# Performance work log

Hardware: AMD Instinct MI355X
Metric: run time of the kernel (lower is better)

Reference implementation:

```python
import jax, jax.numpy as jnp
import numpy as np

D = 256  # feature_dim
NQ = 512
NK = 512


def setup_inputs() -> dict:
    key = jax.random.key(0)
    ks = jax.random.split(key, 12)
    s = 0.05
    return {
        "x": jax.random.normal(ks[0], (1, D, NQ), dtype=jnp.float32),
        "source": jax.random.normal(ks[1], (1, D, NK), dtype=jnp.float32),
        "dist": jax.random.normal(ks[2], (1, D, NQ * NK), dtype=jnp.float32),
        "mask": jax.random.randint(ks[3], (NQ, NK), 0, 2).astype(jnp.bool_),
        # MLPAttention mlp: channels [3D, D, 1] (1x1 convs == per-position matmuls)
        "aW1": jax.random.normal(ks[4], (D, 3 * D), dtype=jnp.float32) * s,
        "ab1": jax.random.normal(ks[5], (D,), dtype=jnp.float32) * s,
        "aW2": jax.random.normal(ks[6], (1, D), dtype=jnp.float32) * s,
        "ab2": jax.random.normal(ks[7], (1,), dtype=jnp.float32) * s,
        # merge mlp: channels [2D, 2D, D], last bias initialized to 0
        "mW1": jax.random.normal(ks[8], (2 * D, 2 * D), dtype=jnp.float32) * s,
        "mb1": jax.random.normal(ks[9], (2 * D,), dtype=jnp.float32) * s,
        "mW2": jax.random.normal(ks[10], (D, 2 * D), dtype=jnp.float32) * s,
        "mb2": jnp.zeros((D,), dtype=jnp.float32),
    }


def _conv1x1(W, b, x):
    # Conv1d(kernel_size=1): (out,in) @ (b,in,n) -> (b,out,n)
    return jnp.einsum('oc,bcn->bon', W, x) + b[None, :, None]


def reference(x, source, dist, mask, aW1, ab1, aW2, ab2, mW1, mb1, mW2, mb2):
    nq, nk = x.shape[-1], source.shape[-1]
    d = x.shape[1]
    # broadcast query over keys and key over queries, flatten to (1, d, nq*nk)
    qb = jnp.broadcast_to(x[:, :, :, None], (1, d, nq, nk)).reshape(1, d, nq * nk)
    kb = jnp.broadcast_to(source[:, :, None, :], (1, d, nq, nk)).reshape(1, d, nq * nk)
    feat = jnp.concatenate([qb, kb, dist], axis=1)  # (1, 3d, nq*nk)
    h = jax.nn.relu(_conv1x1(aW1, ab1, feat))       # (1, d, nq*nk)
    scores = _conv1x1(aW2, ab2, h).reshape(1, nq, nk)
    # boolean-mask branch: push masked-out entries far below the min
    neg = jax.lax.stop_gradient(scores.min()) - 20.0
    scores = scores + neg * (~mask).astype(scores.dtype)[None]
    prob = jax.nn.softmax(scores, axis=-1)
    message = jnp.einsum('bnm,bdm->bdn', prob, source)  # value == source
    # merge MLP on concat([x, message])
    cat = jnp.concatenate([x, message], axis=1)  # (1, 2d, nq)
    h2 = jax.nn.relu(_conv1x1(mW1, mb1, cat))
    out = _conv1x1(mW2, mb2, h2)  # (1, d, nq)
    return (out, scores)
```

## Files before the change

kernel.cpp:

```cpp
#include <hip/hip_runtime.h>
#include <stdint.h>

#define D_ 256
#define NQ_ 512
#define NK_ 512
#define NP_ (NQ_*NK_)

typedef __attribute__((ext_vector_type(8))) __bf16 bf16x8;
typedef __attribute__((ext_vector_type(4))) float f32x4;

__device__ __forceinline__ unsigned short f2bf(float f) {
  unsigned u = __builtin_bit_cast(unsigned, f);
  u += 0x7FFFu + ((u >> 16) & 1u);
  return (unsigned short)(u >> 16);
}
__device__ __forceinline__ unsigned encf(float f) {
  unsigned u = __builtin_bit_cast(unsigned, f);
  return (u & 0x80000000u) ? ~u : (u | 0x80000000u);
}
__device__ __forceinline__ float decf(unsigned e) {
  unsigned u = (e & 0x80000000u) ? (e ^ 0x80000000u) : ~e;
  return __builtin_bit_cast(float, u);
}

template<int EPI, int KTILES>
__device__ __forceinline__ void gemm_body(
    const unsigned short* __restrict__ A, int lda,
    const unsigned short* __restrict__ B, int ldb,
    const float* __restrict__ bias,
    void* __restrict__ Dst, int ldd, int nTilesN, int bid) {
  const int t = threadIdx.x, w = t >> 6, l = t & 63, l15 = l & 15, g = l >> 4;
  const int bm = bid / nTilesN, bn = bid % nTilesN;
  const int m0 = bm*64 + w*16, n0 = bn*64;
  const unsigned short* Ap = A + (size_t)(m0 + l15)*lda + g*8;
  const unsigned short* Bp = B + (size_t)(n0 + l15)*ldb + g*8;
  f32x4 acc[4];
  #pragma unroll
  for (int n = 0; n < 4; ++n) acc[n] = (f32x4){0.f,0.f,0.f,0.f};
  #pragma unroll 2
  for (int kk = 0; kk < KTILES; ++kk) {
    bf16x8 a = *(const bf16x8*)(Ap + kk*32);
    #pragma unroll
    for (int n = 0; n < 4; ++n) {
      bf16x8 b = *(const bf16x8*)(Bp + (size_t)n*16*ldb + kk*32);
      acc[n] = __builtin_amdgcn_mfma_f32_16x16x32_bf16(a, b, acc[n], 0, 0, 0);
    }
  }
  #pragma unroll
  for (int n = 0; n < 4; ++n) {
    const int col = n0 + n*16 + l15;
    const float bc = (EPI & 4) ? bias[col] : 0.f;
    #pragma unroll
    for (int r = 0; r < 4; ++r) {
      const int m = m0 + g*4 + r;
      float v = acc[n][r] + bc;
      if (EPI & 8) v += bias[m];
      if (EPI & 2) v = fmaxf(v, 0.f);
      if (EPI & 1) ((unsigned short*)Dst)[(size_t)m*ldd + col] = f2bf(v);
      else         ((float*)Dst)[(size_t)m*ldd + col] = v;
    }
  }
}

template<int EPI, int KTILES>
__global__ __launch_bounds__(256) void gemm_k(
    const unsigned short* __restrict__ A, int lda,
    const unsigned short* __restrict__ B, int ldb,
    const float* __restrict__ bias,
    void* __restrict__ Dst, int ldd, int nTilesN) {
  gemm_body<EPI, KTILES>(A, lda, B, ldb, bias, Dst, ldd, nTilesN, blockIdx.x);
}

__global__ __launch_bounds__(256) void kprep(
    const unsigned* __restrict__ maskw, unsigned* __restrict__ wsMin,
    unsigned* __restrict__ wsFlag,
    const float* __restrict__ aW1, const float* __restrict__ source,
    const float* __restrict__ x, const float* __restrict__ mW1,
    const float* __restrict__ mW2,
    unsigned short* __restrict__ Cb, unsigned short* __restrict__ srcbf,
    unsigned short* __restrict__ mW1b, unsigned short* __restrict__ mW2b,
    unsigned short* __restrict__ aW1A, unsigned short* __restrict__ aW1B,
    unsigned short* __restrict__ catT, unsigned short* __restrict__ srcT) {
  __shared__ float tile[64][65];
  const int b = blockIdx.x, t = threadIdx.x;
  if (b == 0) {
    if (t < 64) {
      unsigned a01 = 1, af = 1;
      for (int i = 0; i < 4; ++i) {
        unsigned v = maskw[t*4 + i];
        a01 &= (v == 0u || v == 1u) ? 1u : 0u;
        af  &= (v == 0u || v == 0x3f800000u) ? 1u : 0u;
      }
      unsigned long long b01 = __ballot(a01 != 0), bf = __ballot(af != 0);
      if (t == 0) {
        *wsFlag = (b01 == ~0ull) ? 1u : ((bf == ~0ull) ? 2u : 0u);
        *wsMin = 0xFFFFFFFFu;
      }
    }
    return;
  }
  if (b < 705) {
    const int bb = b - 1;
    const float* src; unsigned short* dst;
    if (bb < 64)        { int j = bb*1024 + t*4;       int e=j>>8, c=j&255; src = aW1 + e*768 + 512 + c; dst = Cb + j; }
    else if (bb < 192)  { int j = (bb-64)*1024 + t*4;  src = source + j;    dst = srcbf + j; }
    else if (bb < 448)  { int j = (bb-192)*1024 + t*4; src = mW1 + j;       dst = mW1b + j; }
    else if (bb < 576)  { int j = (bb-448)*1024 + t*4; src = mW2 + j;       dst = mW2b + j; }
    else if (bb < 640)  { int j = (bb-576)*1024 + t*4; int e=j>>8, c=j&255; src = aW1 + e*768 + c;       dst = aW1A + j; }
    else                { int j = (bb-640)*1024 + t*4; int e=j>>8, c=j&255; src = aW1 + e*768 + 256 + c; dst = aW1B + j; }
    const float4 v = *(const float4*)src;
    ushort4 o; o.x=f2bf(v.x); o.y=f2bf(v.y); o.z=f2bf(v.z); o.w=f2bf(v.w);
    *(ushort4*)dst = o;
    return;
  }
  const float* src; unsigned short* dst; int ldd, bid;
  if (b < 737) { src = x;      dst = catT; ldd = 512; bid = b - 705; }
  else         { src = source; dst = srcT; ldd = 256; bid = b - 737; }
  const int bd = bid >> 3, bq = bid & 7;
  const int r = t >> 4, c4 = (t & 15) * 4;
  #pragma unroll
  for (int rr = 0; rr < 4; ++rr) {
    int dl = rr*16 + r;
    float4 v = *(const float4*)(src + (size_t)(bd*64 + dl)*512 + bq*64 + c4);
    tile[dl][c4+0] = v.x; tile[dl][c4+1] = v.y; tile[dl][c4+2] = v.z; tile[dl][c4+3] = v.w;
  }
  __syncthreads();
  #pragma unroll
  for (int rr = 0; rr < 4; ++rr) {
    int j = rr*16 + r;
    ushort4 o;
    o.x = f2bf(tile[c4+0][j]); o.y = f2bf(tile[c4+1][j]);
    o.z = f2bf(tile[c4+2][j]); o.w = f2bf(tile[c4+3][j]);
    *(ushort4*)(dst + (size_t)(bq*64 + j)*ldd + bd*64 + c4) = o;
  }
}

__global__ __launch_bounds__(256) void kprep2(
    const unsigned short* __restrict__ catT, const unsigned short* __restrict__ aW1A,
    const float* __restrict__ ab1, float* __restrict__ Up,
    const unsigned short* __restrict__ aW1B, const unsigned short* __restrict__ srcT,
    float* __restrict__ Vm) {
  if (blockIdx.x < 32)
    gemm_body<4, 8>(catT, 512, aW1A, 256, ab1, (void*)Up, 256, 4, blockIdx.x);
  else
    gemm_body<0, 8>(aW1B, 256, srcT, 256, (const float*)nullptr, (void*)Vm, 512, 8, blockIdx.x - 32);
}

__device__ __forceinline__ void loads8(float (&s)[8], const float* __restrict__ dbase,
                                       int kk, int quad1, int quad2) {
  #pragma unroll
  for (int i = 0; i < 4; ++i) s[i]   = dbase[(size_t)(kk*32 + quad1*4 + i) * NP_];
  #pragma unroll
  for (int i = 0; i < 4; ++i) s[4+i] = dbase[(size_t)(kk*32 + quad2*4 + i) * NP_];
}
__device__ __forceinline__ void cvtwrite(unsigned char* __restrict__ buf, const float (&s)[8],
                                         int l, int quad1, int quad2) {
  const int key = (l >> 1) & 3;
  {
    unsigned lo = (unsigned)f2bf(s[0]) | ((unsigned)f2bf(s[1]) << 16);
    unsigned hi = (unsigned)f2bf(s[2]) | ((unsigned)f2bf(s[3]) << 16);
    *(uint2*)(buf + l*64 + ((((quad1>>1) ^ key) << 4) | ((quad1 & 1) << 3))) = make_uint2(lo, hi);
  }
  {
    unsigned lo = (unsigned)f2bf(s[4]) | ((unsigned)f2bf(s[5]) << 16);
    unsigned hi = (unsigned)f2bf(s[6]) | ((unsigned)f2bf(s[7]) << 16);
    *(uint2*)(buf + l*64 + ((((quad2>>1) ^ key) << 4) | ((quad2 & 1) << 3))) = make_uint2(lo, hi);
  }
}
__device__ __forceinline__ void loadA(bf16x8 (&a)[4], const unsigned short* __restrict__ Abase,
                                      int kk) {
  #pragma unroll
  for (int m = 0; m < 4; ++m)
    a[m] = *(const bf16x8*)(Abase + (size_t)m*16*256 + kk*32);
}
__device__ __forceinline__ void computeStep(f32x4 (&acc)[4][4], const bf16x8 (&a)[4],
                                            const unsigned char* __restrict__ buf,
                                            int l15, int g) {
  bf16x8 bfrag[4];
  #pragma unroll
  for (int n = 0; n < 4; ++n) {
    const int p = n*16 + l15;
    bfrag[n] = *(const bf16x8*)(buf + p*64 + ((g ^ ((p >> 1) & 3)) << 4));
  }
  #pragma unroll
  for (int m = 0; m < 4; ++m)
    #pragma unroll
    for (int n = 0; n < 4; ++n)
      acc[m][n] = __builtin_amdgcn_mfma_f32_16x16x32_bf16(a[m], bfrag[n], acc[m][n], 0, 0, 0);
}

__global__ __launch_bounds__(256, 3) void kscores(
    const float* __restrict__ dist, const unsigned short* __restrict__ Cb,
    const float* __restrict__ Up, const float* __restrict__ Vm,
    const float* __restrict__ aW2, const float* __restrict__ ab2,
    float* __restrict__ outScores, unsigned* __restrict__ wsMin) {
  __shared__ __align__(16) unsigned char ldsB[2][64*64];
  __shared__ float u_s[256], aw2_s[256];
  __shared__ float red[4][64];

  const int t = threadIdx.x;
  const int w = t >> 6;
  const int l = t & 63;
  const int l15 = l & 15;
  const int g = l >> 4;

  const int bid = blockIdx.x;
  const int p0 = ((bid & 7) * 512 + (bid >> 3)) * 64;
  const int q  = p0 >> 9;
  const int k0 = p0 & 511;

  const int quad1 = (w + g) & 3;
  const int quad2 = quad1 + 4;

  const float* dbase = dist + (size_t)p0 + l;
  const unsigned short* Abase = Cb + (size_t)(w*64 + l15)*256 + g*8;

  const float upv = Up[q*256 + t];
  const float awv = aW2[t];
  u_s[t]   = upv;
  aw2_s[t] = awv;
  __builtin_amdgcn_sched_barrier(0);

  float s[3][8];
  loads8(s[0], dbase, 0, quad1, quad2);
  loads8(s[1], dbase, 1, quad1, quad2);
  loads8(s[2], dbase, 2, quad1, quad2);
  bf16x8 af[2][4];
  loadA(af[0], Abase, 0);

  f32x4 acc[4][4];
  #pragma unroll
  for (int m = 0; m < 4; ++m)
    #pragma unroll
    for (int n = 0; n < 4; ++n) acc[m][n] = (f32x4){0.f, 0.f, 0.f, 0.f};

  #pragma unroll
  for (int kk = 0; kk < 8; ++kk) {
    const int b = kk & 1;
    cvtwrite(ldsB[b], s[kk % 3], l, quad1, quad2);
    if (kk < 5) loads8(s[kk % 3], dbase, kk + 3, quad1, quad2);
    __builtin_amdgcn_sched_barrier(0);
    asm volatile("s_waitcnt lgkmcnt(0)" ::: "memory");
    __builtin_amdgcn_s_barrier();
    __builtin_amdgcn_sched_barrier(0);
    if (kk < 7) loadA(af[(kk + 1) & 1], Abase, kk + 1);
    computeStep(acc, af[b], ldsB[b], l15, g);
  }

  float part[4];
  #pragma unroll
  for (int n = 0; n < 4; ++n) {
    int j = k0 + n*16 + l15;
    float s2 = 0.f;
    #pragma unroll
    for (int m = 0; m < 4; ++m) {
      #pragma unroll
      for (int r = 0; r < 4; ++r) {
        int e = w*64 + m*16 + g*4 + r;
        float gv = acc[m][n][r] + u_s[e] + Vm[e*512 + j];
        s2 += aw2_s[e] * fmaxf(gv, 0.f);
      }
    }
    s2 += __shfl_xor(s2, 16);
    s2 += __shfl_xor(s2, 32);
    part[n] = s2;
  }
  if (l < 16) {
    #pragma unroll
    for (int n = 0; n < 4; ++n) red[w][n*16 + l] = part[n];
  }
  __syncthreads();
  if (t < 64) {
    float s2 = red[0][t] + red[1][t] + red[2][t] + red[3][t] + ab2[0];
    outScores[p0 + t] = s2;
    float mn = s2;
    #pragma unroll
    for (int off = 32; off; off >>= 1) mn = fminf(mn, __shfl_xor(mn, off));
    if (t == 0) atomicMin(wsMin, encf(mn));
  }
}

__global__ __launch_bounds__(256) void ksoftmax(
    const void* __restrict__ maskp,
    const unsigned* __restrict__ wsMin, const unsigned* __restrict__ wsFlag,
    float* __restrict__ scores, unsigned short* __restrict__ prob) {
  __shared__ float srow[512];
  __shared__ float redl[8];
  const int t = threadIdx.x, w = t >> 6, l = t & 63;
  const int q = blockIdx.x;
  const float neg = decf(*wsMin) - 20.0f;
  const unsigned flag = *wsFlag;

  for (int k = t; k < 512; k += 256) {
    float raw = scores[q*512 + k];
    bool mv;
    if (flag == 1)      mv = ((const int*)maskp)[q*512 + k] != 0;
    else if (flag == 2) mv = ((const float*)maskp)[q*512 + k] != 0.f;
    else                mv = ((const unsigned char*)maskp)[q*512 + k] != 0;
    float ms = raw + (mv ? 0.f : neg);
    scores[q*512 + k] = ms;
    srow[k] = ms;
  }
  __syncthreads();
  float lm = fmaxf(srow[t], srow[t + 256]);
  #pragma unroll
  for (int off = 32; off; off >>= 1) lm = fmaxf(lm, __shfl_xor(lm, off));
  if (l == 0) redl[w] = lm;
  __syncthreads();
  float rmax = fmaxf(fmaxf(redl[0], redl[1]), fmaxf(redl[2], redl[3]));
  float e0 = __expf(srow[t] - rmax), e1 = __expf(srow[t + 256] - rmax);
  float ls = e0 + e1;
  #pragma unroll
  for (int off = 32; off; off >>= 1) ls += __shfl_xor(ls, off);
  if (l == 0) redl[4 + w] = ls;
  __syncthreads();
  float inv = 1.0f / (redl[4] + redl[5] + redl[6] + redl[7]);
  prob[q*512 + t]       = f2bf(e0 * inv);
  prob[q*512 + t + 256] = f2bf(e1 * inv);
}

extern "C" void kernel_launch(void* const* d_in, const int* in_sizes, int n_in,
                              void* d_out, int out_size, void* d_ws, size_t ws_size,
                              hipStream_t stream) {
  const float* x      = (const float*)d_in[0];
  const float* source = (const float*)d_in[1];
  const float* dist   = (const float*)d_in[2];
  const void*  mask   = (const void*)d_in[3];
  const float* aW1    = (const float*)d_in[4];
  const float* ab1    = (const float*)d_in[5];
  const float* aW2    = (const float*)d_in[6];
  const float* ab2    = (const float*)d_in[7];
  const float* mW1    = (const float*)d_in[8];
  const float* mb1    = (const float*)d_in[9];
  const float* mW2    = (const float*)d_in[10];
  const float* mb2    = (const float*)d_in[11];

  float* outMain = (float*)d_out;
  float* scores  = outMain + 256*512;

  char* ws = (char*)d_ws;
  unsigned* wsMin  = (unsigned*)ws;
  unsigned* wsFlag = wsMin + 1;
  unsigned short* Cb    = (unsigned short*)(ws + 1024);
  float*          Up    = (float*)(ws + 132096);
  float*          Vm    = (float*)(ws + 656384);
  unsigned short* srcbf = (unsigned short*)(ws + 1180672);
  unsigned short* srcT  = (unsigned short*)(ws + 1442816);
  unsigned short* mW1b  = (unsigned short*)(ws + 1704960);
  unsigned short* mW2b  = (unsigned short*)(ws + 2229248);
  unsigned short* aW1A  = (unsigned short*)(ws + 2491392);
  unsigned short* aW1B  = (unsigned short*)(ws + 2622464);
  unsigned short* catT  = (unsigned short*)(ws + 2753536);
  unsigned short* prob  = (unsigned short*)(ws + 3277824);
  unsigned short* h2T   = (unsigned short*)(ws + 3802112);

  hipLaunchKernelGGL(kprep, dim3(769), dim3(256), 0, stream,
                     (const unsigned*)mask, wsMin, wsFlag, aW1, source, x, mW1, mW2,
                     Cb, srcbf, mW1b, mW2b, aW1A, aW1B, catT, srcT);
  hipLaunchKernelGGL(kprep2, dim3(64), dim3(256), 0, stream,
                     catT, aW1A, ab1, Up, aW1B, srcT, Vm);
  hipLaunchKernelGGL(kscores, dim3(4096), dim3(256), 0, stream,
                     dist, Cb, Up, Vm, aW2, ab2, scores, wsMin);
  hipLaunchKernelGGL(ksoftmax, dim3(512), dim3(256), 0, stream,
                     mask, wsMin, wsFlag, scores, prob);
  hipLaunchKernelGGL((gemm_k<1, 16>), dim3(32), dim3(256), 0, stream,
                     prob, 512, srcbf, 512, (const float*)nullptr, (void*)(catT + 256), 512, 4);
  hipLaunchKernelGGL((gemm_k<7, 16>), dim3(64), dim3(256), 0, stream,
                     catT, 512, mW1b, 512, mb1, (void*)h2T, 512, 8);
  hipLaunchKernelGGL((gemm_k<8, 16>), dim3(32), dim3(256), 0, stream,
                     mW2b, 512, h2T, 512, mb2, (void*)outMain, 512, 8);
}
```

Baseline: 206.3 us.

## Pre-transpose dist into bf16 MFMA-fragment images in a separate kernel

A new kernel reads dist (256 channels x 262144 positions, fp32) with wide coalesced float4 loads, transposes it through LDS, converts it to bf16 and writes per-tile fragment images to a workspace buffer. The scores kernel then loads those images with one 16-byte load per thread and copies them straight into LDS. The aW1 dist slice is also pre-permuted into MFMA A-fragment order. This replaces strided scalar fp32 gathers and in-kernel conversion, at the cost of an extra launch and a 128MB bf16 intermediate that is written and then read back.

```diff
diff --git a/kernel.cpp b/kernel.cpp
--- a/kernel.cpp
+++ b/kernel.cpp
@@ -77,7 +77,7 @@
     const float* __restrict__ aW1, const float* __restrict__ source,
     const float* __restrict__ x, const float* __restrict__ mW1,
     const float* __restrict__ mW2,
-    unsigned short* __restrict__ Cb, unsigned short* __restrict__ srcbf,
+    unsigned short* __restrict__ Ab, unsigned short* __restrict__ srcbf,
     unsigned short* __restrict__ mW1b, unsigned short* __restrict__ mW2b,
     unsigned short* __restrict__ aW1A, unsigned short* __restrict__ aW1B,
     unsigned short* __restrict__ catT, unsigned short* __restrict__ srcT) {
@@ -102,7 +102,13 @@
   if (b < 705) {
     const int bb = b - 1;
     const float* src; unsigned short* dst;
-    if (bb < 64)        { int j = bb*1024 + t*4;       int e=j>>8, c=j&255; src = aW1 + e*768 + 512 + c; dst = Cb + j; }
+    if (bb < 64) {
+      int j = bb*1024 + t*4;
+      int img = j >> 9, li = (j >> 3) & 63, i0 = j & 7;
+      int row = ((img >> 2) & 3)*64 + (img & 3)*16 + (li & 15);
+      int ch  = (img >> 4)*32 + (li >> 4)*8 + i0;
+      src = aW1 + row*768 + 512 + ch; dst = Ab + j;
+    }
     else if (bb < 192)  { int j = (bb-64)*1024 + t*4;  src = source + j;    dst = srcbf + j; }
     else if (bb < 448)  { int j = (bb-192)*1024 + t*4; src = mW1 + j;       dst = mW1b + j; }
     else if (bb < 576)  { int j = (bb-448)*1024 + t*4; src = mW2 + j;       dst = mW2b + j; }
@@ -146,87 +152,78 @@
     gemm_body<0, 8>(aW1B, 256, srcT, 256, (const float*)nullptr, (void*)Vm, 512, 8, blockIdx.x - 32);
 }
 
-__device__ __forceinline__ void loads8(float (&s)[8], const float* __restrict__ dbase,
-                                       int kk, int quad1, int quad2) {
-  #pragma unroll
-  for (int i = 0; i < 4; ++i) s[i]   = dbase[(size_t)(kk*32 + quad1*4 + i) * NP_];
-  #pragma unroll
-  for (int i = 0; i < 4; ++i) s[4+i] = dbase[(size_t)(kk*32 + quad2*4 + i) * NP_];
-}
-__device__ __forceinline__ void cvtwrite(unsigned char* __restrict__ buf, const float (&s)[8],
-                                         int l, int quad1, int quad2) {
-  const int key = (l >> 1) & 3;
-  {
-    unsigned lo = (unsigned)f2bf(s[0]) | ((unsigned)f2bf(s[1]) << 16);
-    unsigned hi = (unsigned)f2bf(s[2]) | ((unsigned)f2bf(s[3]) << 16);
-    *(uint2*)(buf + l*64 + ((((quad1>>1) ^ key) << 4) | ((quad1 & 1) << 3))) = make_uint2(lo, hi);
-  }
-  {
-    unsigned lo = (unsigned)f2bf(s[4]) | ((unsigned)f2bf(s[5]) << 16);
-    unsigned hi = (unsigned)f2bf(s[6]) | ((unsigned)f2bf(s[7]) << 16);
-    *(uint2*)(buf + l*64 + ((((quad2>>1) ^ key) << 4) | ((quad2 & 1) << 3))) = make_uint2(lo, hi);
-  }
-}
-__device__ __forceinline__ void loadA(bf16x8 (&a)[4], const unsigned short* __restrict__ Abase,
-                                      int kk) {
-  #pragma unroll
-  for (int m = 0; m < 4; ++m)
-    a[m] = *(const bf16x8*)(Abase + (size_t)m*16*256 + kk*32);
-}
-__device__ __forceinline__ void computeStep(f32x4 (&acc)[4][4], const bf16x8 (&a)[4],
-                                            const unsigned char* __restrict__ buf,
-                                            int l15, int g) {
-  bf16x8 bfrag[4];
-  #pragma unroll
-  for (int n = 0; n < 4; ++n) {
-    const int p = n*16 + l15;
-    bfrag[n] = *(const bf16x8*)(buf + p*64 + ((g ^ ((p >> 1) & 3)) << 4));
-  }
-  #pragma unroll
-  for (int m = 0; m < 4; ++m)
-    #pragma unroll
-    for (int n = 0; n < 4; ++n)
-      acc[m][n] = __builtin_amdgcn_mfma_f32_16x16x32_bf16(a[m], bfrag[n], acc[m][n], 0, 0, 0);
-}
-
-__global__ __launch_bounds__(256, 3) void kscores(
-    const float* __restrict__ dist, const unsigned short* __restrict__ Cb,
+__global__ __launch_bounds__(256) void ktrans(const float* __restrict__ dist,
+                                              unsigned short* __restrict__ Bt) {
+  __shared__ float ld[32*514];
+  const int t = threadIdx.x, w = t >> 6, l = t & 63;
+  const int cb = blockIdx.x & 3;
+  const int pb = blockIdx.x >> 2;
+  const size_t p0g = (size_t)pb * 2048;
+  for (int h = 0; h < 2; ++h) {
+    const int kk = cb*2 + h;
+    const int c0 = cb*64 + h*32;
+    for (int pc = 0; pc < 4; ++pc) {
+      float4 v[16];
+      #pragma unroll
+      for (int i = 0; i < 16; ++i) {
+        const int chl = w*8 + (i >> 1);
+        v[i] = *(const float4*)(dist + (size_t)(c0 + chl)*NP_ + p0g + pc*512 + (i&1)*256 + l*4);
+      }
+      #pragma unroll
+      for (int i = 0; i < 16; ++i) {
+        const int chl = w*8 + (i >> 1);
+        const int pl = (i&1)*256 + l*4;
+        *(float2*)(&ld[chl*514 + pl])     = make_float2(v[i].x, v[i].y);
+        *(float2*)(&ld[chl*514 + pl + 2]) = make_float2(v[i].z, v[i].w);
+      }
+      __syncthreads();
+      #pragma unroll
+      for (int ii = 0; ii < 2; ++ii) {
+        const int ptl = w*2 + ii;
+        const size_t pt = (size_t)pb*32 + pc*8 + ptl;
+        unsigned short* dst = Bt + (pt*8 + kk)*2048;
+        const int g = l >> 4;
+        #pragma unroll
+        for (int n = 0; n < 4; ++n) {
+          const int pl = ptl*64 + n*16 + (l & 15);
+          unsigned q0 = (unsigned)f2bf(ld[(g*8+0)*514 + pl]) | ((unsigned)f2bf(ld[(g*8+1)*514 + pl]) << 16);
+          unsigned q1 = (unsigned)f2bf(ld[(g*8+2)*514 + pl]) | ((unsigned)f2bf(ld[(g*8+3)*514 + pl]) << 16);
+          unsigned q2 = (unsigned)f2bf(ld[(g*8+4)*514 + pl]) | ((unsigned)f2bf(ld[(g*8+5)*514 + pl]) << 16);
+          unsigned q3 = (unsigned)f2bf(ld[(g*8+6)*514 + pl]) | ((unsigned)f2bf(ld[(g*8+7)*514 + pl]) << 16);
+          *(uint4*)(dst + n*512 + l*8) = make_uint4(q0, q1, q2, q3);
+        }
+      }
+      __syncthreads();
+    }
+  }
+}
+
+__global__ __launch_bounds__(256, 3) void kscores2(
+    const unsigned short* __restrict__ Bt, const unsigned short* __restrict__ Ab,
     const float* __restrict__ Up, const float* __restrict__ Vm,
     const float* __restrict__ aW2, const float* __restrict__ ab2,
     float* __restrict__ outScores, unsigned* __restrict__ wsMin) {
-  __shared__ __align__(16) unsigned char ldsB[2][64*64];
+  __shared__ __align__(16) unsigned char ldsB[2][4096];
   __shared__ float u_s[256], aw2_s[256];
   __shared__ float red[4][64];
 
-  const int t = threadIdx.x;
-  const int w = t >> 6;
-  const int l = t & 63;
-  const int l15 = l & 15;
-  const int g = l >> 4;
-
+  const int t = threadIdx.x, w = t >> 6, l = t & 63, l15 = l & 15, g = l >> 4;
   const int bid = blockIdx.x;
-  const int p0 = ((bid & 7) * 512 + (bid >> 3)) * 64;
-  const int q  = p0 >> 9;
-  const int k0 = p0 & 511;
-
-  const int quad1 = (w + g) & 3;
-  const int quad2 = quad1 + 4;
-
-  const float* dbase = dist + (size_t)p0 + l;
-  const unsigned short* Abase = Cb + (size_t)(w*64 + l15)*256 + g*8;
-
-  const float upv = Up[q*256 + t];
-  const float awv = aW2[t];
-  u_s[t]   = upv;
-  aw2_s[t] = awv;
-  __builtin_amdgcn_sched_barrier(0);
-
-  float s[3][8];
-  loads8(s[0], dbase, 0, quad1, quad2);
-  loads8(s[1], dbase, 1, quad1, quad2);
-  loads8(s[2], dbase, 2, quad1, quad2);
+  const int pt = (bid & 7) * 512 + (bid >> 3);
+  const int p0 = pt * 64;
+  const int q = p0 >> 9, k0 = p0 & 511;
+  const unsigned short* img = Bt + (size_t)pt * 16384;
+
+  u_s[t]   = Up[q*256 + t];
+  aw2_s[t] = aW2[t];
+
+  uint4 bs[2];
+  bs[0] = *(const uint4*)(img + 0*2048 + t*8);
+  bs[1] = *(const uint4*)(img + 1*2048 + t*8);
   bf16x8 af[2][4];
-  loadA(af[0], Abase, 0);
+  #pragma unroll
+  for (int m = 0; m < 4; ++m)
+    af[0][m] = *(const bf16x8*)(Ab + (size_t)(w*4 + m)*512 + l*8);
 
   f32x4 acc[4][4];
   #pragma unroll
@@ -237,14 +234,26 @@
   #pragma unroll
   for (int kk = 0; kk < 8; ++kk) {
     const int b = kk & 1;
-    cvtwrite(ldsB[b], s[kk % 3], l, quad1, quad2);
-    if (kk < 5) loads8(s[kk % 3], dbase, kk + 3, quad1, quad2);
+    *(uint4*)(&ldsB[b][t*16]) = bs[b];
+    if (kk < 6) bs[b] = *(const uint4*)(img + (size_t)(kk+2)*2048 + t*8);
+    if (kk < 7) {
+      #pragma unroll
+      for (int m = 0; m < 4; ++m)
+        af[(kk+1)&1][m] = *(const bf16x8*)(Ab + (size_t)((kk+1)*16 + w*4 + m)*512 + l*8);
+    }
     __builtin_amdgcn_sched_barrier(0);
     asm volatile("s_waitcnt lgkmcnt(0)" ::: "memory");
     __builtin_amdgcn_s_barrier();
     __builtin_amdgcn_sched_barrier(0);
-    if (kk < 7) loadA(af[(kk + 1) & 1], Abase, kk + 1);
-    computeStep(acc, af[b], ldsB[b], l15, g);
+    bf16x8 bfrag[4];
+    #pragma unroll
+    for (int n = 0; n < 4; ++n)
+      bfrag[n] = *(const bf16x8*)(&ldsB[b][n*1024 + l*16]);
+    #pragma unroll
+    for (int m = 0; m < 4; ++m)
+      #pragma unroll
+      for (int n = 0; n < 4; ++n)
+        acc[m][n] = __builtin_amdgcn_mfma_f32_16x16x32_bf16(af[b][m], bfrag[n], acc[m][n], 0, 0, 0);
   }
 
   float part[4];
@@ -341,7 +350,7 @@
   char* ws = (char*)d_ws;
   unsigned* wsMin  = (unsigned*)ws;
   unsigned* wsFlag = wsMin + 1;
-  unsigned short* Cb    = (unsigned short*)(ws + 1024);
+  unsigned short* Ab    = (unsigned short*)(ws + 1024);
   float*          Up    = (float*)(ws + 132096);
   float*          Vm    = (float*)(ws + 656384);
   unsigned short* srcbf = (unsigned short*)(ws + 1180672);
@@ -353,14 +362,16 @@
   unsigned short* catT  = (unsigned short*)(ws + 2753536);
   unsigned short* prob  = (unsigned short*)(ws + 3277824);
   unsigned short* h2T   = (unsigned short*)(ws + 3802112);
+  unsigned short* Bt    = (unsigned short*)(ws + 16*1024*1024);
 
   hipLaunchKernelGGL(kprep, dim3(769), dim3(256), 0, stream,
                      (const unsigned*)mask, wsMin, wsFlag, aW1, source, x, mW1, mW2,
-                     Cb, srcbf, mW1b, mW2b, aW1A, aW1B, catT, srcT);
+                     Ab, srcbf, mW1b, mW2b, aW1A, aW1B, catT, srcT);
   hipLaunchKernelGGL(kprep2, dim3(64), dim3(256), 0, stream,
                      catT, aW1A, ab1, Up, aW1B, srcT, Vm);
-  hipLaunchKernelGGL(kscores, dim3(4096), dim3(256), 0, stream,
-                     dist, Cb, Up, Vm, aW2, ab2, scores, wsMin);
+  hipLaunchKernelGGL(ktrans, dim3(512), dim3(256), 0, stream, dist, Bt);
+  hipLaunchKernelGGL(kscores2, dim3(4096), dim3(256), 0, stream,
+                     Bt, Ab, Up, Vm, aW2, ab2, scores, wsMin);
   hipLaunchKernelGGL(ksoftmax, dim3(512), dim3(256), 0, stream,
                      mask, wsMin, wsFlag, scores, prob);
   hipLaunchKernelGGL((gemm_k<1, 16>), dim3(32), dim3(256), 0, stream,
```

Result: slower. 228.3 us (+10.7%).

## Make scores kernel persistent over four tiles with cross-tile dist prefetch

Applied to the files above, without the earlier changes.

The scores kernel now runs 1024 blocks, each processing four consecutive 64-position tiles, and prefetches the next tile's dist data during the last k-steps of the current tile so the load pipeline stays full across tiles. The aW1 C-slice is pre-swizzled into an MFMA-fragment layout so each lane reads one contiguous 16-byte chunk. Vm is stored transposed so the epilogue can use float4 loads. Up is folded into the accumulator initial value, and aW2 is kept in registers instead of LDS. The cost is higher register pressure (occupancy hint drops from 3 to 2) and fewer blocks to spread over the GPU.

```diff
diff --git a/kernel.cpp b/kernel.cpp
--- a/kernel.cpp
+++ b/kernel.cpp
@@ -77,7 +77,7 @@
     const float* __restrict__ aW1, const float* __restrict__ source,
     const float* __restrict__ x, const float* __restrict__ mW1,
     const float* __restrict__ mW2,
-    unsigned short* __restrict__ Cb, unsigned short* __restrict__ srcbf,
+    unsigned short* __restrict__ Ab, unsigned short* __restrict__ srcbf,
     unsigned short* __restrict__ mW1b, unsigned short* __restrict__ mW2b,
     unsigned short* __restrict__ aW1A, unsigned short* __restrict__ aW1B,
     unsigned short* __restrict__ catT, unsigned short* __restrict__ srcT) {
@@ -102,7 +102,13 @@
   if (b < 705) {
     const int bb = b - 1;
     const float* src; unsigned short* dst;
-    if (bb < 64)        { int j = bb*1024 + t*4;       int e=j>>8, c=j&255; src = aW1 + e*768 + 512 + c; dst = Cb + j; }
+    if (bb < 64) {
+      int j = bb*1024 + t*4;
+      int img = j >> 9, li = (j >> 3) & 63, i0 = j & 7;
+      int row = ((img >> 2) & 3)*64 + (img & 3)*16 + (li & 15);
+      int ch  = (img >> 4)*32 + (li >> 4)*8 + i0;
+      src = aW1 + row*768 + 512 + ch; dst = Ab + j;
+    }
     else if (bb < 192)  { int j = (bb-64)*1024 + t*4;  src = source + j;    dst = srcbf + j; }
     else if (bb < 448)  { int j = (bb-192)*1024 + t*4; src = mW1 + j;       dst = mW1b + j; }
     else if (bb < 576)  { int j = (bb-448)*1024 + t*4; src = mW2 + j;       dst = mW2b + j; }
@@ -138,12 +144,12 @@
 __global__ __launch_bounds__(256) void kprep2(
     const unsigned short* __restrict__ catT, const unsigned short* __restrict__ aW1A,
     const float* __restrict__ ab1, float* __restrict__ Up,
-    const unsigned short* __restrict__ aW1B, const unsigned short* __restrict__ srcT,
-    float* __restrict__ Vm) {
+    const unsigned short* __restrict__ srcT, const unsigned short* __restrict__ aW1B,
+    float* __restrict__ VmT) {
   if (blockIdx.x < 32)
     gemm_body<4, 8>(catT, 512, aW1A, 256, ab1, (void*)Up, 256, 4, blockIdx.x);
   else
-    gemm_body<0, 8>(aW1B, 256, srcT, 256, (const float*)nullptr, (void*)Vm, 512, 8, blockIdx.x - 32);
+    gemm_body<0, 8>(srcT, 256, aW1B, 256, (const float*)nullptr, (void*)VmT, 256, 4, blockIdx.x - 32);
 }
 
 __device__ __forceinline__ void loads8(float (&s)[8], const float* __restrict__ dbase,
@@ -167,11 +173,11 @@
     *(uint2*)(buf + l*64 + ((((quad2>>1) ^ key) << 4) | ((quad2 & 1) << 3))) = make_uint2(lo, hi);
   }
 }
-__device__ __forceinline__ void loadA(bf16x8 (&a)[4], const unsigned short* __restrict__ Abase,
-                                      int kk) {
+__device__ __forceinline__ void loadA(bf16x8 (&a)[4], const unsigned short* __restrict__ Ab,
+                                      int kk, int w, int l) {
   #pragma unroll
   for (int m = 0; m < 4; ++m)
-    a[m] = *(const bf16x8*)(Abase + (size_t)m*16*256 + kk*32);
+    a[m] = *(const bf16x8*)(Ab + ((kk*16 + w*4 + m) << 9) + l*8);
 }
 __device__ __forceinline__ void computeStep(f32x4 (&acc)[4][4], const bf16x8 (&a)[4],
                                             const unsigned char* __restrict__ buf,
@@ -189,94 +195,105 @@
       acc[m][n] = __builtin_amdgcn_mfma_f32_16x16x32_bf16(a[m], bfrag[n], acc[m][n], 0, 0, 0);
 }
 
-__global__ __launch_bounds__(256, 3) void kscores(
-    const float* __restrict__ dist, const unsigned short* __restrict__ Cb,
-    const float* __restrict__ Up, const float* __restrict__ Vm,
+__global__ __launch_bounds__(256, 2) void kscores3(
+    const float* __restrict__ dist, const unsigned short* __restrict__ Ab,
+    const float* __restrict__ VmT, const float* __restrict__ Up,
     const float* __restrict__ aW2, const float* __restrict__ ab2,
     float* __restrict__ outScores, unsigned* __restrict__ wsMin) {
-  __shared__ __align__(16) unsigned char ldsB[2][64*64];
-  __shared__ float u_s[256], aw2_s[256];
+  __shared__ __align__(16) unsigned char ldsB[2][4096];
   __shared__ float red[4][64];
 
-  const int t = threadIdx.x;
-  const int w = t >> 6;
-  const int l = t & 63;
-  const int l15 = l & 15;
-  const int g = l >> 4;
-
-  const int bid = blockIdx.x;
-  const int p0 = ((bid & 7) * 512 + (bid >> 3)) * 64;
-  const int q  = p0 >> 9;
-  const int k0 = p0 & 511;
+  const int t = threadIdx.x, w = t >> 6, l = t & 63, l15 = l & 15, g = l >> 4;
+  const int bs = (blockIdx.x & 7) * 128 + (blockIdx.x >> 3);
+  const int base_tile = bs * 4;
 
   const int quad1 = (w + g) & 3;
   const int quad2 = quad1 + 4;
 
-  const float* dbase = dist + (size_t)p0 + l;
-  const unsigned short* Abase = Cb + (size_t)(w*64 + l15)*256 + g*8;
-
-  const float upv = Up[q*256 + t];
-  const float awv = aW2[t];
-  u_s[t]   = upv;
-  aw2_s[t] = awv;
-  __builtin_amdgcn_sched_barrier(0);
-
-  float s[3][8];
-  loads8(s[0], dbase, 0, quad1, quad2);
-  loads8(s[1], dbase, 1, quad1, quad2);
-  loads8(s[2], dbase, 2, quad1, quad2);
-  bf16x8 af[2][4];
-  loadA(af[0], Abase, 0);
-
-  f32x4 acc[4][4];
-  #pragma unroll
-  for (int m = 0; m < 4; ++m)
-    #pragma unroll
-    for (int n = 0; n < 4; ++n) acc[m][n] = (f32x4){0.f, 0.f, 0.f, 0.f};
-
-  #pragma unroll
-  for (int kk = 0; kk < 8; ++kk) {
-    const int b = kk & 1;
-    cvtwrite(ldsB[b], s[kk % 3], l, quad1, quad2);
-    if (kk < 5) loads8(s[kk % 3], dbase, kk + 3, quad1, quad2);
-    __builtin_amdgcn_sched_barrier(0);
+  float aw[4][4];
+  #pragma unroll
+  for (int m = 0; m < 4; ++m) {
+    const float4 v = *(const float4*)(aW2 + w*64 + m*16 + g*4);
+    aw[m][0]=v.x; aw[m][1]=v.y; aw[m][2]=v.z; aw[m][3]=v.w;
+  }
+  const float ab2v = ab2[0];
+
+  float s[4][8];
+  {
+    const float* db0 = dist + (size_t)base_tile*64 + l;
+    loads8(s[0], db0, 0, quad1, quad2);
+    loads8(s[1], db0, 1, quad1, quad2);
+    loads8(s[2], db0, 2, quad1, quad2);
+  }
+
+  for (int tt = 0; tt < 4; ++tt) {
+    const int p0 = (base_tile + tt) * 64;
+    const int q  = p0 >> 9;
+    const int k0 = p0 & 511;
+    const float* dbase = dist + (size_t)p0 + l;
+
+    f32x4 acc[4][4];
+    #pragma unroll
+    for (int m = 0; m < 4; ++m) {
+      const float4 u = *(const float4*)(Up + q*256 + w*64 + m*16 + g*4);
+      #pragma unroll
+      for (int n = 0; n < 4; ++n) {
+        acc[m][n][0]=u.x; acc[m][n][1]=u.y; acc[m][n][2]=u.z; acc[m][n][3]=u.w;
+      }
+    }
+
+    bf16x8 af[2][4];
+    loadA(af[0], Ab, 0, w, l);
+
+    #pragma unroll
+    for (int kk = 0; kk < 8; ++kk) {
+      const int bb = kk & 1;
+      cvtwrite(ldsB[bb], s[kk & 3], l, quad1, quad2);
+      if (kk < 5) {
+        loads8(s[(kk + 3) & 3], dbase, kk + 3, quad1, quad2);
+      } else if (tt < 3) {
+        loads8(s[(kk + 3) & 3], dbase + 64, kk - 5, quad1, quad2);
+      }
+      __builtin_amdgcn_sched_barrier(0);
+      asm volatile("s_waitcnt lgkmcnt(0)" ::: "memory");
+      __builtin_amdgcn_s_barrier();
+      __builtin_amdgcn_sched_barrier(0);
+      if (kk < 7) loadA(af[(kk + 1) & 1], Ab, kk + 1, w, l);
+      computeStep(acc, af[kk & 1], ldsB[bb], l15, g);
+    }
+
+    float part[4];
+    #pragma unroll
+    for (int n = 0; n < 4; ++n) {
+      const int j = k0 + n*16 + l15;
+      float s2 = 0.f;
+      #pragma unroll
+      for (int m = 0; m < 4; ++m) {
+        const float4 v4 = *(const float4*)(VmT + (size_t)j*256 + w*64 + m*16 + g*4);
+        s2 += aw[m][0] * fmaxf(acc[m][n][0] + v4.x, 0.f);
+        s2 += aw[m][1] * fmaxf(acc[m][n][1] + v4.y, 0.f);
+        s2 += aw[m][2] * fmaxf(acc[m][n][2] + v4.z, 0.f);
+        s2 += aw[m][3] * fmaxf(acc[m][n][3] + v4.w, 0.f);
+      }
+      s2 += __shfl_xor(s2, 16);
+      s2 += __shfl_xor(s2, 32);
+      part[n] = s2;
+    }
+    __builtin_amdgcn_s_barrier();
+    if (l < 16) {
+      #pragma unroll
+      for (int n = 0; n < 4; ++n) red[w][n*16 + l] = part[n];
+    }
     asm volatile("s_waitcnt lgkmcnt(0)" ::: "memory");
     __builtin_amdgcn_s_barrier();
-    __builtin_amdgcn_sched_barrier(0);
-    if (kk < 7) loadA(af[(kk + 1) & 1], Abase, kk + 1);
-    computeStep(acc, af[b], ldsB[b], l15, g);
-  }
-
-  float part[4];
-  #pragma unroll
-  for (int n = 0; n < 4; ++n) {
-    int j = k0 + n*16 + l15;
-    float s2 = 0.f;
-    #pragma unroll
-    for (int m = 0; m < 4; ++m) {
+    if (t < 64) {
+      float s2 = red[0][t] + red[1][t] + red[2][t] + red[3][t] + ab2v;
+      outScores[p0 + t] = s2;
+      float mn = s2;
       #pragma unroll
-      for (int r = 0; r < 4; ++r) {
-        int e = w*64 + m*16 + g*4 + r;
-        float gv = acc[m][n][r] + u_s[e] + Vm[e*512 + j];
-        s2 += aw2_s[e] * fmaxf(gv, 0.f);
-      }
-    }
-    s2 += __shfl_xor(s2, 16);
-    s2 += __shfl_xor(s2, 32);
-    part[n] = s2;
-  }
-  if (l < 16) {
-    #pragma unroll
-    for (int n = 0; n < 4; ++n) red[w][n*16 + l] = part[n];
-  }
-  __syncthreads();
-  if (t < 64) {
-    float s2 = red[0][t] + red[1][t] + red[2][t] + red[3][t] + ab2[0];
-    outScores[p0 + t] = s2;
-    float mn = s2;
-    #pragma unroll
-    for (int off = 32; off; off >>= 1) mn = fminf(mn, __shfl_xor(mn, off));
-    if (t == 0) atomicMin(wsMin, encf(mn));
+      for (int off = 32; off; off >>= 1) mn = fminf(mn, __shfl_xor(mn, off));
+      if (t == 0) atomicMin(wsMin, encf(mn));
+    }
   }
 }
 
@@ -341,9 +358,9 @@
   char* ws = (char*)d_ws;
   unsigned* wsMin  = (unsigned*)ws;
   unsigned* wsFlag = wsMin + 1;
-  unsigned short* Cb    = (unsigned short*)(ws + 1024);
+  unsigned short* Ab    = (unsigned short*)(ws + 1024);
   float*          Up    = (float*)(ws + 132096);
-  float*          Vm    = (float*)(ws + 656384);
+  float*          VmT   = (float*)(ws + 656384);
   unsigned short* srcbf = (unsigned short*)(ws + 1180672);
   unsigned short* srcT  = (unsigned short*)(ws + 1442816);
   unsigned short* mW1b  = (unsigned short*)(ws + 1704960);
@@ -356,11 +373,11 @@
 
   hipLaunchKernelGGL(kprep, dim3(769), dim3(256), 0, stream,
                      (const unsigned*)mask, wsMin, wsFlag, aW1, source, x, mW1, mW2,
-                     Cb, srcbf, mW1b, mW2b, aW1A, aW1B, catT, srcT);
+                     Ab, srcbf, mW1b, mW2b, aW1A, aW1B, catT, srcT);
   hipLaunchKernelGGL(kprep2, dim3(64), dim3(256), 0, stream,
-                     catT, aW1A, ab1, Up, aW1B, srcT, Vm);
-  hipLaunchKernelGGL(kscores, dim3(4096), dim3(256), 0, stream,
-                     dist, Cb, Up, Vm, aW2, ab2, scores, wsMin);
+                     catT, aW1A, ab1, Up, srcT, aW1B, VmT);
+  hipLaunchKernelGGL(kscores3, dim3(1024), dim3(256), 0, stream,
+                     dist, Ab, VmT, Up, aW2, ab2, scores, wsMin);
   hipLaunchKernelGGL(ksoftmax, dim3(512), dim3(256), 0, stream,
                      mask, wsMin, wsFlag, scores, prob);
   hipLaunchKernelGGL((gemm_k<1, 16>), dim3(32), dim3(256), 0, stream,
```

Result: faster. 167.1 us (median of 3 runs) (-19.0%).
